# Kernel optimization log

Hardware: AMD Instinct MI355X
Metric: run time of the kernel (lower is better)

Reference implementation:

```python
import jax, jax.numpy as jnp
import numpy as np

N, E = 50000, 800000
IN, HID, OUT = 128, 256, 40
EPS = 1e-5


def setup_inputs() -> dict:
    key = jax.random.key(0)
    ks = jax.random.split(key, 16)
    def glorot(k, shape):
        lim = float(np.sqrt(6.0 / (shape[0] + shape[1])))
        return jax.random.uniform(k, shape, jnp.float32, -lim, lim)
    return {
        "x": jax.random.normal(ks[0], (N, IN), jnp.float32),
        "edge_index": jax.random.randint(ks[1], (2, E), 0, N, jnp.int64),
        "W1": glorot(ks[2], (IN, HID)),  "b1": jnp.zeros((HID,), jnp.float32),
        "g1": jnp.ones((HID,), jnp.float32), "be1": jnp.zeros((HID,), jnp.float32),
        "W2": glorot(ks[3], (HID, HID)), "b2": jnp.zeros((HID,), jnp.float32),
        "g2": jnp.ones((HID,), jnp.float32), "be2": jnp.zeros((HID,), jnp.float32),
        "W3": glorot(ks[4], (HID, OUT)), "b3": jnp.zeros((OUT,), jnp.float32),
        "Wl": glorot(ks[5], (OUT, OUT)), "bl": jnp.zeros((OUT,), jnp.float32),
    }


def _gcn_conv(h, src, dst, norm, W, b, n):
    # PyG GCNConv: transform, then normalized scatter-add over edges (+self-loops)
    m = h @ W                                     # [N, d_out]
    msg = m[src] * norm[:, None]                  # gather + edge scale
    out = jax.ops.segment_sum(msg, dst, num_segments=n)
    return out + b


def _bn(h, g, b):
    # BatchNorm1d (training-mode batch stats, biased variance)
    mu = jnp.mean(h, axis=0)
    var = jnp.var(h, axis=0)
    return (h - mu) * jax.lax.rsqrt(var + EPS) * g + b


def reference(x, edge_index, W1, b1, g1, be1, W2, b2, g2, be2, W3, b3, Wl, bl):
    n = x.shape[0]
    loops = jnp.arange(n, dtype=edge_index.dtype)
    src = jnp.concatenate([edge_index[0], loops])
    dst = jnp.concatenate([edge_index[1], loops])
    deg = jax.ops.segment_sum(jnp.ones(src.shape[0], x.dtype), dst, num_segments=n)
    dinv = jnp.where(deg > 0, jax.lax.rsqrt(deg), 0.0)
    norm = dinv[src] * dinv[dst]

    h = jax.nn.relu(_bn(_gcn_conv(x, src, dst, norm, W1, b1, n), g1, be1))
    h = jax.nn.relu(_bn(_gcn_conv(h, src, dst, norm, W2, b2, n), g2, be2))
    h = _gcn_conv(h, src, dst, norm, W3, b3, n)
    h = h @ Wl + bl
    return jax.nn.log_softmax(h, axis=1)
```

## Files before the change

kernel.cpp:

```cpp
#include <hip/hip_runtime.h>
#include <hip/hip_bf16.h>
#include <math.h>

#define IN_DIM 128
#define HID 256
#define OUT_DIM 40
#define OUT_PAD 64
#define CAP 64
#define EPS 1e-5f

typedef __attribute__((ext_vector_type(8))) short short8;
typedef __attribute__((ext_vector_type(4))) float floatx4;

__device__ __forceinline__ float b2f(unsigned short u) {
    union { unsigned int i; float f; } c; c.i = ((unsigned int)u) << 16; return c.f;
}
__device__ __forceinline__ unsigned short f2b(float f) {
    union { float f; unsigned int i; } c; c.f = f;
    unsigned int r = c.i + 0x7FFF + ((c.i >> 16) & 1);
    return (unsigned short)(r >> 16);
}

union U8 { uint4 u; unsigned short s[8]; };
union F8 { short8 v; unsigned short s[8]; uint4 u; };


__global__ void fill1_k(const int* __restrict__ src, const int* __restrict__ dst,
                        int* __restrict__ cnt, int* __restrict__ col2, int E,
                        const float* __restrict__ W1, const float* __restrict__ W2,
                        const float* __restrict__ W3, const float* __restrict__ Wl,
                        const float* __restrict__ b3, const float* __restrict__ bl,
                        unsigned short* __restrict__ W1t, unsigned short* __restrict__ W2t,
                        unsigned short* __restrict__ W3lt, float* __restrict__ bias2,
                        float* __restrict__ stats1, float* __restrict__ stats2) {
    if (blockIdx.x < 1024) {
        for (int e = blockIdx.x * 256 + threadIdx.x; e < E; e += 1024 * 256) {
            int d = dst[e];
            int p = atomicAdd(&cnt[d], 1);
            if (p < CAP) col2[d * CAP + p] = src[e];
        }
    } else if (blockIdx.x < 1536) {
        const int n1 = 256 * 128, n2 = 256 * 256;
        int j = (blockIdx.x - 1024) * 256 + threadIdx.x;
        if (j < n1) {
            int n = j >> 7, k = j & 127;
            W1t[j] = f2b(W1[k * 256 + n]);
        } else if (j < n1 + n2) {
            int j2 = j - n1;
            int n = j2 >> 8, k = j2 & 255;
            W2t[j2] = f2b(W2[k * 256 + n]);
        } else {
            int j3 = j - n1 - n2;
            int n = j3 >> 8, k = j3 & 255;
            float acc = 0.f;
            if (n < OUT_DIM) {
                for (int q = 0; q < OUT_DIM; ++q)
                    acc += W3[k * OUT_DIM + q] * Wl[q * OUT_DIM + n];
            }
            W3lt[j3] = (n < OUT_DIM) ? f2b(acc) : 0;
            if (j3 < OUT_DIM) {
                float b = bl[j3];
                for (int q = 0; q < OUT_DIM; ++q) b += b3[q] * Wl[q * OUT_DIM + j3];
                bias2[j3] = b;
            }
        }
    } else {
        int t = threadIdx.x;
        stats1[t] = 0.f; stats1[256 + t] = 0.f;
        stats2[t] = 0.f; stats2[256 + t] = 0.f;
    }
}


__global__ void conv_k(const float* __restrict__ x, const int* __restrict__ cnt,
                       float* __restrict__ dinv, unsigned short* __restrict__ xb, int N) {
    size_t nx = (size_t)N * 32;
    for (size_t i = blockIdx.x * 256 + threadIdx.x; i < nx; i += (size_t)1024 * 256) {
        size_t row = i >> 5;
        float dv = rsqrtf((float)(cnt[row] + 1));
        if ((i & 31) == 0) dinv[row] = dv;
        float4 v = ((const float4*)x)[i];
        ushort4 o;
        o.x = f2b(v.x * dv); o.y = f2b(v.y * dv);
        o.z = f2b(v.z * dv); o.w = f2b(v.w * dv);
        ((ushort4*)xb)[i] = o;
    }
}


template <bool BN>
__global__ __launch_bounds__(64, 3) void gemm_w(const unsigned short* __restrict__ A,
                                                const unsigned short* __restrict__ Bt,
                                                unsigned short* __restrict__ C,
                                                const float* __restrict__ rowscale,
                                                const float* __restrict__ bias,
                                                const float* __restrict__ bnstats,
                                                const float* __restrict__ g,
                                                const float* __restrict__ be,
                                                float invN,
                                                int M, int Nc, int K, int ldc) {
    __shared__ float s_sc[HID], s_sh[HID];
    int lane = threadIdx.x;
    if (BN) {
        for (int t = lane; t < K; t += 64) {
            float mu = bnstats[t] * invN;
            float var = bnstats[HID + t] * invN - mu * mu;
            float sc = g[t] * rsqrtf(var + EPS);
            s_sc[t] = sc;
            s_sh[t] = be[t] - mu * sc;
        }
        __syncthreads();
    }
    int r16 = lane & 15, quad = lane >> 4;
    int row0 = blockIdx.y * 64, col0 = blockIdx.x * 64;

    int arow[4];
#pragma unroll
    for (int mt = 0; mt < 4; ++mt) arow[mt] = min(row0 + mt * 16 + r16, M - 1);

    floatx4 acc[4][4] = {};

    for (int k0 = 0; k0 < K; k0 += 32) {
        int ka = k0 + quad * 8;
        F8 a[4], b[4];
#pragma unroll
        for (int mt = 0; mt < 4; ++mt)
            a[mt].u = *(const uint4*)&A[(size_t)arow[mt] * K + ka];
#pragma unroll
        for (int nt = 0; nt < 4; ++nt)
            b[nt].u = *(const uint4*)&Bt[(size_t)(col0 + nt * 16 + r16) * K + ka];
        if (BN) {
            float4 sc0 = *(const float4*)&s_sc[ka];
            float4 sc1 = *(const float4*)&s_sc[ka + 4];
            float4 sh0 = *(const float4*)&s_sh[ka];
            float4 sh1 = *(const float4*)&s_sh[ka + 4];
            float sc[8] = {sc0.x, sc0.y, sc0.z, sc0.w, sc1.x, sc1.y, sc1.z, sc1.w};
            float sh[8] = {sh0.x, sh0.y, sh0.z, sh0.w, sh1.x, sh1.y, sh1.z, sh1.w};
#pragma unroll
            for (int mt = 0; mt < 4; ++mt)
#pragma unroll
                for (int j = 0; j < 8; ++j) {
                    float f = b2f(a[mt].s[j]) * sc[j] + sh[j];
                    a[mt].s[j] = f2b(fmaxf(f, 0.f));
                }
        }
#pragma unroll
        for (int mt = 0; mt < 4; ++mt)
#pragma unroll
            for (int nt = 0; nt < 4; ++nt)
                acc[mt][nt] = __builtin_amdgcn_mfma_f32_16x16x32_bf16(a[mt].v, b[nt].v, acc[mt][nt], 0, 0, 0);
    }

#pragma unroll
    for (int mt = 0; mt < 4; ++mt) {
#pragma unroll
        for (int r = 0; r < 4; ++r) {
            int row = row0 + mt * 16 + quad * 4 + r;
            if (row >= M) continue;
            float dv = rowscale ? rowscale[row] : 1.f;
#pragma unroll
            for (int nt = 0; nt < 4; ++nt) {
                int colg = col0 + nt * 16 + r16;
                if (colg < Nc) {
                    float v = acc[mt][nt][r] * dv + (bias ? bias[colg] : 0.f);
                    C[(size_t)row * ldc + colg] = f2b(v);
                }
            }
        }
    }
}


__global__ __launch_bounds__(256, 8) void agg_h(const unsigned short* __restrict__ m,
                                                const int* __restrict__ col2,
                                                const int* __restrict__ cnt,
                                                const float* __restrict__ dinv,
                                                const float* __restrict__ bias,
                                                unsigned short* __restrict__ out,
                                                int N) {
    int v = blockIdx.x * 4 + (threadIdx.x >> 6);
    if (v >= N) return;
    int lane = threadIdx.x & 63;
    int half = lane >> 5;
    int c0 = (lane & 31) * 8;
    float dv = dinv[v];
    const int* col = col2 + v * CAP;
    int end = min(cnt[v], CAP);
    float a[8] = {};
    if (half == 0) {
        U8 r; r.u = *(const uint4*)&m[(size_t)v * HID + c0];
#pragma unroll
        for (int k = 0; k < 8; ++k) a[k] = b2f(r.s[k]);
    }
    int e = 0;
    for (; e + 8 <= end; e += 8) {
        int idx[4];
#pragma unroll
        for (int j = 0; j < 4; ++j) idx[j] = col[e + 2 * j + half];
        U8 rr[4];
#pragma unroll
        for (int j = 0; j < 4; ++j)
            rr[j].u = *(const uint4*)&m[(size_t)idx[j] * HID + c0];
#pragma unroll
        for (int j = 0; j < 4; ++j)
#pragma unroll
            for (int k = 0; k < 8; ++k) a[k] += b2f(rr[j].s[k]);
    }
    for (; e < end; e += 2) {
        int t = e + half;
        if (t < end) {
            U8 r; r.u = *(const uint4*)&m[(size_t)col[t] * HID + c0];
#pragma unroll
            for (int k = 0; k < 8; ++k) a[k] += b2f(r.s[k]);
        }
    }
#pragma unroll
    for (int k = 0; k < 8; ++k) a[k] += __shfl_xor(a[k], 32);
    if (half == 0) {
        U8 o;
#pragma unroll
        for (int k = 0; k < 8; ++k) o.s[k] = f2b(a[k] * dv + bias[c0 + k]);
        *(uint4*)&out[(size_t)v * HID + c0] = o.u;
    }
}

__global__ __launch_bounds__(256, 8) void agg_x(const unsigned short* __restrict__ m,
                                                const int* __restrict__ col2,
                                                const int* __restrict__ cnt,
                                                const float* __restrict__ dinv,
                                                unsigned short* __restrict__ out,
                                                int N) {
    int v = blockIdx.x * 4 + (threadIdx.x >> 6);
    if (v >= N) return;
    int lane = threadIdx.x & 63;
    int q = lane >> 4;
    int c0 = (lane & 15) * 8;
    float dv = dinv[v];
    const int* col = col2 + v * CAP;
    int end = min(cnt[v], CAP);
    float a[8] = {};
    if (q == 0) {
        U8 r; r.u = *(const uint4*)&m[(size_t)v * IN_DIM + c0];
#pragma unroll
        for (int k = 0; k < 8; ++k) a[k] = b2f(r.s[k]);
    }
    int e = 0;
    for (; e + 8 <= end; e += 8) {
        int idx[2];
#pragma unroll
        for (int j = 0; j < 2; ++j) idx[j] = col[e + 4 * j + q];
        U8 rr[2];
#pragma unroll
        for (int j = 0; j < 2; ++j)
            rr[j].u = *(const uint4*)&m[(size_t)idx[j] * IN_DIM + c0];
#pragma unroll
        for (int j = 0; j < 2; ++j)
#pragma unroll
            for (int k = 0; k < 8; ++k) a[k] += b2f(rr[j].s[k]);
    }
    for (; e < end; e += 4) {
        int t = e + q;
        if (t < end) {
            U8 r; r.u = *(const uint4*)&m[(size_t)col[t] * IN_DIM + c0];
#pragma unroll
            for (int k = 0; k < 8; ++k) a[k] += b2f(r.s[k]);
        }
    }
#pragma unroll
    for (int k = 0; k < 8; ++k) {
        a[k] += __shfl_xor(a[k], 16);
        a[k] += __shfl_xor(a[k], 32);
    }
    if (q == 0) {
        U8 o;
#pragma unroll
        for (int k = 0; k < 8; ++k) o.s[k] = f2b(a[k] * dv);
        *(uint4*)&out[(size_t)v * IN_DIM + c0] = o.u;
    }
}

__global__ __launch_bounds__(256, 8) void agg_o_ls(const unsigned short* __restrict__ m,
                                                   const int* __restrict__ col2,
                                                   const int* __restrict__ cnt,
                                                   const float* __restrict__ dinv,
                                                   const float* __restrict__ bias2,
                                                   float* __restrict__ out,
                                                   int N) {
    int v = blockIdx.x * 4 + (threadIdx.x >> 6);
    if (v >= N) return;
    int lane = threadIdx.x & 63;
    int slot = lane >> 3;
    int li = lane & 7;
    int c0 = li * 8;
    float dv = dinv[v];
    const int* col = col2 + v * CAP;
    int end = min(cnt[v], CAP);
    float a[8] = {};
    if (slot == 0) {
        U8 r; r.u = *(const uint4*)&m[(size_t)v * OUT_PAD + c0];
#pragma unroll
        for (int k = 0; k < 8; ++k) a[k] = b2f(r.s[k]);
    }
    int e = 0;
    for (; e + 16 <= end; e += 16) {
        int idx[2];
        idx[0] = col[e + slot];
        idx[1] = col[e + 8 + slot];
        U8 rr[2];
#pragma unroll
        for (int j = 0; j < 2; ++j)
            rr[j].u = *(const uint4*)&m[(size_t)idx[j] * OUT_PAD + c0];
#pragma unroll
        for (int j = 0; j < 2; ++j)
#pragma unroll
            for (int k = 0; k < 8; ++k) a[k] += b2f(rr[j].s[k]);
    }
    for (; e < end; e += 8) {
        int t = e + slot;
        if (t < end) {
            U8 r; r.u = *(const uint4*)&m[(size_t)col[t] * OUT_PAD + c0];
#pragma unroll
            for (int k = 0; k < 8; ++k) a[k] += b2f(r.s[k]);
        }
    }
#pragma unroll
    for (int k = 0; k < 8; ++k) {
        a[k] += __shfl_xor(a[k], 8);
        a[k] += __shfl_xor(a[k], 16);
        a[k] += __shfl_xor(a[k], 32);
    }
    bool valid = (li < 5);
    float mx = -INFINITY;
#pragma unroll
    for (int k = 0; k < 8; ++k) {
        float val = valid ? (a[k] * dv + bias2[c0 + k]) : -INFINITY;
        a[k] = val;
        mx = fmaxf(mx, val);
    }
    mx = fmaxf(mx, __shfl_xor(mx, 1));
    mx = fmaxf(mx, __shfl_xor(mx, 2));
    mx = fmaxf(mx, __shfl_xor(mx, 4));
    float s = 0.f;
    if (valid) {
#pragma unroll
        for (int k = 0; k < 8; ++k) s += expf(a[k] - mx);
    }
    s += __shfl_xor(s, 1);
    s += __shfl_xor(s, 2);
    s += __shfl_xor(s, 4);
    float ls = mx + logf(s);
    if (slot == 0 && valid) {
        float4 o0, o1;
        o0.x = a[0] - ls; o0.y = a[1] - ls; o0.z = a[2] - ls; o0.w = a[3] - ls;
        o1.x = a[4] - ls; o1.y = a[5] - ls; o1.z = a[6] - ls; o1.w = a[7] - ls;
        float* p = &out[(size_t)v * OUT_DIM + c0];
        *(float4*)p = o0;
        *(float4*)(p + 4) = o1;
    }
}


__global__ __launch_bounds__(256) void bn_stats(const unsigned short* __restrict__ h,
                                                float* __restrict__ stats, int N) {
    __shared__ float ls[8][2][256];
    int t = threadIdx.x;
    int walker = t >> 5;
    int c0 = (t & 31) * 8;
    int r0 = blockIdx.x * 128;
    int rend = min(r0 + 128, N);
    float s1[8] = {}, s2[8] = {};
    for (int r = r0 + walker; r < rend; r += 8) {
        U8 x; x.u = *(const uint4*)&h[(size_t)r * HID + c0];
#pragma unroll
        for (int k = 0; k < 8; ++k) {
            float v = b2f(x.s[k]);
            s1[k] += v; s2[k] += v * v;
        }
    }
#pragma unroll
    for (int k = 0; k < 8; ++k) {
        ls[walker][0][c0 + k] = s1[k];
        ls[walker][1][c0 + k] = s2[k];
    }
    __syncthreads();
    float a1 = 0.f, a2 = 0.f;
#pragma unroll
    for (int w = 0; w < 8; ++w) { a1 += ls[w][0][t]; a2 += ls[w][1][t]; }
    atomicAdd(&stats[t], a1);
    atomicAdd(&stats[HID + t], a2);
}


extern "C" void kernel_launch(void* const* d_in, const int* in_sizes, int n_in,
                              void* d_out, int out_size, void* d_ws, size_t ws_size,
                              hipStream_t stream) {
    const float* x   = (const float*)d_in[0];
    const int*  eidx = (const int*)d_in[1];
    const float* W1 = (const float*)d_in[2];
    const float* b1 = (const float*)d_in[3];
    const float* g1 = (const float*)d_in[4];
    const float* be1 = (const float*)d_in[5];
    const float* W2 = (const float*)d_in[6];
    const float* b2 = (const float*)d_in[7];
    const float* g2 = (const float*)d_in[8];
    const float* be2 = (const float*)d_in[9];
    const float* W3 = (const float*)d_in[10];
    const float* b3 = (const float*)d_in[11];
    const float* Wl = (const float*)d_in[12];
    const float* bl = (const float*)d_in[13];
    float* out = (float*)d_out;

    const int N = in_sizes[0] / IN_DIM;
    const int E = in_sizes[1] / 2;
    const int* src = eidx;
    const int* dst = eidx + E;

    size_t off = 0;
    char* ws = (char*)d_ws;
    auto carve = [&](size_t bytes) -> void* {
        void* p = ws + off;
        off += (bytes + 255) & ~(size_t)255;
        return p;
    };
    int*   cnt  = (int*)carve((size_t)N * 4);
    float* stats1 = (float*)carve((size_t)2 * HID * 4);
    float* stats2 = (float*)carve((size_t)2 * HID * 4);
    float* dinv = (float*)carve((size_t)N * 4);
    int*   col2 = (int*)carve((size_t)N * CAP * 4);
    unsigned short* xb   = (unsigned short*)carve((size_t)N * IN_DIM * 2);
    unsigned short* axb  = (unsigned short*)carve((size_t)N * IN_DIM * 2);
    unsigned short* W1t  = (unsigned short*)carve((size_t)256 * IN_DIM * 2);
    unsigned short* W2t  = (unsigned short*)carve((size_t)256 * HID * 2);
    unsigned short* W3lt = (unsigned short*)carve((size_t)128 * HID * 2);
    float* bias2 = (float*)carve((size_t)OUT_DIM * 4);
    unsigned short* mbuf = (unsigned short*)carve((size_t)N * HID * 2);
    unsigned short* hbuf = (unsigned short*)carve((size_t)N * HID * 2);

    hipMemsetAsync(cnt, 0, (size_t)N * 4, stream);
    fill1_k<<<1537, 256, 0, stream>>>(src, dst, cnt, col2, E,
                                      W1, W2, W3, Wl, b3, bl,
                                      W1t, W2t, W3lt, bias2, stats1, stats2);
    conv_k<<<1024, 256, 0, stream>>>(x, cnt, dinv, xb, N);

    int mb64 = (N + 63) / 64;
    int nodeBlocks = (N + 3) / 4;
    float invN = 1.f / (float)N;

    agg_x<<<nodeBlocks, 256, 0, stream>>>(xb, col2, cnt, dinv, axb, N);
    gemm_w<false><<<dim3(4, mb64), 64, 0, stream>>>(axb, W1t, hbuf, nullptr, b1,
                                                    nullptr, nullptr, nullptr,
                                                    invN, N, HID, IN_DIM, HID);
    bn_stats<<<(N + 127) / 128, 256, 0, stream>>>(hbuf, stats1, N);

    gemm_w<true><<<dim3(4, mb64), 64, 0, stream>>>(hbuf, W2t, mbuf, dinv, nullptr,
                                                   stats1, g1, be1,
                                                   invN, N, HID, HID, HID);
    agg_h<<<nodeBlocks, 256, 0, stream>>>(mbuf, col2, cnt, dinv, b2, hbuf, N);
    bn_stats<<<(N + 127) / 128, 256, 0, stream>>>(hbuf, stats2, N);

    gemm_w<true><<<dim3(1, mb64), 64, 0, stream>>>(hbuf, W3lt, mbuf, dinv, nullptr,
                                                   stats2, g2, be2,
                                                   invN, N, OUT_PAD, HID, OUT_PAD);
    agg_o_ls<<<nodeBlocks, 256, 0, stream>>>(mbuf, col2, cnt, dinv, bias2, out, N);
}
```

Measured before the change: 414.6 us.

## Fuse x conversion into setup kernel, BN1 stats into GEMM, smaller GEMM tiles

The separate conv_k pass is removed. The x-to-bf16 conversion now runs as extra blocks of the setup kernel, and the degree scaling is recomputed inside the aggregation kernels from cnt instead of reading a dinv array. The first GEMM now accumulates BatchNorm sums with shuffles and atomics, which removes one bn_stats pass. GEMM row tiles shrink to 32 and 16 rows and the launch-bounds occupancy target rises. The trade-offs are more atomic traffic, extra rsqrt work per gathered neighbour, and BN statistics taken from fp32 values before bf16 rounding.

Result: no change. 422.8 us (+2.0%).

```diff
diff --git a/kernel.cpp b/kernel.cpp
--- a/kernel.cpp
+++ b/kernel.cpp
@@ -32,7 +32,9 @@
                         const float* __restrict__ b3, const float* __restrict__ bl,
                         unsigned short* __restrict__ W1t, unsigned short* __restrict__ W2t,
                         unsigned short* __restrict__ W3lt, float* __restrict__ bias2,
-                        float* __restrict__ stats1, float* __restrict__ stats2) {
+                        float* __restrict__ stats1, float* __restrict__ stats2,
+                        const float* __restrict__ x, unsigned short* __restrict__ xb,
+                        int N) {
     if (blockIdx.x < 1024) {
         for (int e = blockIdx.x * 256 + threadIdx.x; e < E; e += 1024 * 256) {
             int d = dst[e];
@@ -64,42 +66,37 @@
                 bias2[j3] = b;
             }
         }
-    } else {
+    } else if (blockIdx.x == 1536) {
         int t = threadIdx.x;
         stats1[t] = 0.f; stats1[256 + t] = 0.f;
         stats2[t] = 0.f; stats2[256 + t] = 0.f;
-    }
-}
-
-
-__global__ void conv_k(const float* __restrict__ x, const int* __restrict__ cnt,
-                       float* __restrict__ dinv, unsigned short* __restrict__ xb, int N) {
-    size_t nx = (size_t)N * 32;
-    for (size_t i = blockIdx.x * 256 + threadIdx.x; i < nx; i += (size_t)1024 * 256) {
-        size_t row = i >> 5;
-        float dv = rsqrtf((float)(cnt[row] + 1));
-        if ((i & 31) == 0) dinv[row] = dv;
-        float4 v = ((const float4*)x)[i];
-        ushort4 o;
-        o.x = f2b(v.x * dv); o.y = f2b(v.y * dv);
-        o.z = f2b(v.z * dv); o.w = f2b(v.w * dv);
-        ((ushort4*)xb)[i] = o;
-    }
-}
-
-
-template <bool BN>
-__global__ __launch_bounds__(64, 3) void gemm_w(const unsigned short* __restrict__ A,
+    } else {
+        size_t nx = (size_t)N * 32;
+        size_t nbk = gridDim.x - 1537;
+        for (size_t i = (size_t)(blockIdx.x - 1537) * 256 + threadIdx.x; i < nx;
+             i += nbk * 256) {
+            float4 v = ((const float4*)x)[i];
+            ushort4 o;
+            o.x = f2b(v.x); o.y = f2b(v.y); o.z = f2b(v.z); o.w = f2b(v.w);
+            ((ushort4*)xb)[i] = o;
+        }
+    }
+}
+
+
+template <int MT, bool BN, bool STATS>
+__global__ __launch_bounds__(64, 6) void gemm_w(const unsigned short* __restrict__ A,
                                                 const unsigned short* __restrict__ Bt,
                                                 unsigned short* __restrict__ C,
-                                                const float* __restrict__ rowscale,
+                                                const int* __restrict__ cnt,
                                                 const float* __restrict__ bias,
                                                 const float* __restrict__ bnstats,
                                                 const float* __restrict__ g,
                                                 const float* __restrict__ be,
+                                                float* __restrict__ gstats,
                                                 float invN,
                                                 int M, int Nc, int K, int ldc) {
-    __shared__ float s_sc[HID], s_sh[HID];
+    __shared__ float s_sc[BN ? HID : 1], s_sh[BN ? HID : 1];
     int lane = threadIdx.x;
     if (BN) {
         for (int t = lane; t < K; t += 64) {
@@ -112,19 +109,19 @@
         __syncthreads();
     }
     int r16 = lane & 15, quad = lane >> 4;
-    int row0 = blockIdx.y * 64, col0 = blockIdx.x * 64;
-
-    int arow[4];
-#pragma unroll
-    for (int mt = 0; mt < 4; ++mt) arow[mt] = min(row0 + mt * 16 + r16, M - 1);
-
-    floatx4 acc[4][4] = {};
+    int row0 = blockIdx.y * (MT * 16), col0 = blockIdx.x * 64;
+
+    int arow[MT];
+#pragma unroll
+    for (int mt = 0; mt < MT; ++mt) arow[mt] = min(row0 + mt * 16 + r16, M - 1);
+
+    floatx4 acc[MT][4] = {};
 
     for (int k0 = 0; k0 < K; k0 += 32) {
         int ka = k0 + quad * 8;
-        F8 a[4], b[4];
-#pragma unroll
-        for (int mt = 0; mt < 4; ++mt)
+        F8 a[MT], b[4];
+#pragma unroll
+        for (int mt = 0; mt < MT; ++mt)
             a[mt].u = *(const uint4*)&A[(size_t)arow[mt] * K + ka];
 #pragma unroll
         for (int nt = 0; nt < 4; ++nt)
@@ -137,7 +134,7 @@
             float sc[8] = {sc0.x, sc0.y, sc0.z, sc0.w, sc1.x, sc1.y, sc1.z, sc1.w};
             float sh[8] = {sh0.x, sh0.y, sh0.z, sh0.w, sh1.x, sh1.y, sh1.z, sh1.w};
 #pragma unroll
-            for (int mt = 0; mt < 4; ++mt)
+            for (int mt = 0; mt < MT; ++mt)
 #pragma unroll
                 for (int j = 0; j < 8; ++j) {
                     float f = b2f(a[mt].s[j]) * sc[j] + sh[j];
@@ -145,36 +142,110 @@
                 }
         }
 #pragma unroll
-        for (int mt = 0; mt < 4; ++mt)
+        for (int mt = 0; mt < MT; ++mt)
 #pragma unroll
             for (int nt = 0; nt < 4; ++nt)
                 acc[mt][nt] = __builtin_amdgcn_mfma_f32_16x16x32_bf16(a[mt].v, b[nt].v, acc[mt][nt], 0, 0, 0);
     }
 
-#pragma unroll
-    for (int mt = 0; mt < 4; ++mt) {
+    float s1[4] = {0.f, 0.f, 0.f, 0.f}, s2[4] = {0.f, 0.f, 0.f, 0.f};
+#pragma unroll
+    for (int mt = 0; mt < MT; ++mt) {
 #pragma unroll
         for (int r = 0; r < 4; ++r) {
             int row = row0 + mt * 16 + quad * 4 + r;
             if (row >= M) continue;
-            float dv = rowscale ? rowscale[row] : 1.f;
+            float dv = cnt ? rsqrtf((float)(cnt[row] + 1)) : 1.f;
 #pragma unroll
             for (int nt = 0; nt < 4; ++nt) {
                 int colg = col0 + nt * 16 + r16;
                 if (colg < Nc) {
                     float v = acc[mt][nt][r] * dv + (bias ? bias[colg] : 0.f);
                     C[(size_t)row * ldc + colg] = f2b(v);
+                    if (STATS) { s1[nt] += v; s2[nt] += v * v; }
                 }
             }
         }
     }
-}
-
+    if (STATS) {
+#pragma unroll
+        for (int nt = 0; nt < 4; ++nt) {
+            s1[nt] += __shfl_xor(s1[nt], 16); s1[nt] += __shfl_xor(s1[nt], 32);
+            s2[nt] += __shfl_xor(s2[nt], 16); s2[nt] += __shfl_xor(s2[nt], 32);
+            if (quad == 0) {
+                int colg = col0 + nt * 16 + r16;
+                atomicAdd(&gstats[colg], s1[nt]);
+                atomicAdd(&gstats[HID + colg], s2[nt]);
+            }
+        }
+    }
+}
+
+
+__global__ __launch_bounds__(256, 8) void agg_x(const unsigned short* __restrict__ m,
+                                                const int* __restrict__ col2,
+                                                const int* __restrict__ cnt,
+                                                unsigned short* __restrict__ out,
+                                                int N) {
+    int v = blockIdx.x * 4 + (threadIdx.x >> 6);
+    if (v >= N) return;
+    int lane = threadIdx.x & 63;
+    int q = lane >> 4;
+    int c0 = (lane & 15) * 8;
+    int cv = cnt[v];
+    float dv = rsqrtf((float)(cv + 1));
+    const int* col = col2 + v * CAP;
+    int end = min(cv, CAP);
+    float a[8] = {};
+    {
+        U8 r; r.u = *(const uint4*)&m[(size_t)v * IN_DIM + c0];
+#pragma unroll
+        for (int k = 0; k < 8; ++k) a[k] = b2f(r.s[k]) * dv;
+    }
+    if (q != 0) { a[0]=a[1]=a[2]=a[3]=a[4]=a[5]=a[6]=a[7]=0.f; }
+    int e = 0;
+    for (; e + 8 <= end; e += 8) {
+        int idx[2];
+#pragma unroll
+        for (int j = 0; j < 2; ++j) idx[j] = col[e + 4 * j + q];
+        float ds[2];
+#pragma unroll
+        for (int j = 0; j < 2; ++j) ds[j] = rsqrtf((float)(cnt[idx[j]] + 1));
+        U8 rr[2];
+#pragma unroll
+        for (int j = 0; j < 2; ++j)
+            rr[j].u = *(const uint4*)&m[(size_t)idx[j] * IN_DIM + c0];
+#pragma unroll
+        for (int j = 0; j < 2; ++j)
+#pragma unroll
+            for (int k = 0; k < 8; ++k) a[k] += b2f(rr[j].s[k]) * ds[j];
+    }
+    for (; e < end; e += 4) {
+        int t = e + q;
+        if (t < end) {
+            int s = col[t];
+            float ds = rsqrtf((float)(cnt[s] + 1));
+            U8 r; r.u = *(const uint4*)&m[(size_t)s * IN_DIM + c0];
+#pragma unroll
+            for (int k = 0; k < 8; ++k) a[k] += b2f(r.s[k]) * ds;
+        }
+    }
+#pragma unroll
+    for (int k = 0; k < 8; ++k) {
+        a[k] += __shfl_xor(a[k], 16);
+        a[k] += __shfl_xor(a[k], 32);
+    }
+    if (q == 0) {
+        U8 o;
+#pragma unroll
+        for (int k = 0; k < 8; ++k) o.s[k] = f2b(a[k] * dv);
+        *(uint4*)&out[(size_t)v * IN_DIM + c0] = o.u;
+    }
+}
 
 __global__ __launch_bounds__(256, 8) void agg_h(const unsigned short* __restrict__ m,
                                                 const int* __restrict__ col2,
                                                 const int* __restrict__ cnt,
-                                                const float* __restrict__ dinv,
                                                 const float* __restrict__ bias,
                                                 unsigned short* __restrict__ out,
                                                 int N) {
@@ -183,9 +254,10 @@
     int lane = threadIdx.x & 63;
     int half = lane >> 5;
     int c0 = (lane & 31) * 8;
-    float dv = dinv[v];
+    int cv = cnt[v];
+    float dv = rsqrtf((float)(cv + 1));
     const int* col = col2 + v * CAP;
-    int end = min(cnt[v], CAP);
+    int end = min(cv, CAP);
     float a[8] = {};
     if (half == 0) {
         U8 r; r.u = *(const uint4*)&m[(size_t)v * HID + c0];
@@ -224,65 +296,9 @@
     }
 }
 
-__global__ __launch_bounds__(256, 8) void agg_x(const unsigned short* __restrict__ m,
-                                                const int* __restrict__ col2,
-                                                const int* __restrict__ cnt,
-                                                const float* __restrict__ dinv,
-                                                unsigned short* __restrict__ out,
-                                                int N) {
-    int v = blockIdx.x * 4 + (threadIdx.x >> 6);
-    if (v >= N) return;
-    int lane = threadIdx.x & 63;
-    int q = lane >> 4;
-    int c0 = (lane & 15) * 8;
-    float dv = dinv[v];
-    const int* col = col2 + v * CAP;
-    int end = min(cnt[v], CAP);
-    float a[8] = {};
-    if (q == 0) {
-        U8 r; r.u = *(const uint4*)&m[(size_t)v * IN_DIM + c0];
-#pragma unroll
-        for (int k = 0; k < 8; ++k) a[k] = b2f(r.s[k]);
-    }
-    int e = 0;
-    for (; e + 8 <= end; e += 8) {
-        int idx[2];
-#pragma unroll
-        for (int j = 0; j < 2; ++j) idx[j] = col[e + 4 * j + q];
-        U8 rr[2];
-#pragma unroll
-        for (int j = 0; j < 2; ++j)
-            rr[j].u = *(const uint4*)&m[(size_t)idx[j] * IN_DIM + c0];
-#pragma unroll
-        for (int j = 0; j < 2; ++j)
-#pragma unroll
-            for (int k = 0; k < 8; ++k) a[k] += b2f(rr[j].s[k]);
-    }
-    for (; e < end; e += 4) {
-        int t = e + q;
-        if (t < end) {
-            U8 r; r.u = *(const uint4*)&m[(size_t)col[t] * IN_DIM + c0];
-#pragma unroll
-            for (int k = 0; k < 8; ++k) a[k] += b2f(r.s[k]);
-        }
-    }
-#pragma unroll
-    for (int k = 0; k < 8; ++k) {
-        a[k] += __shfl_xor(a[k], 16);
-        a[k] += __shfl_xor(a[k], 32);
-    }
-    if (q == 0) {
-        U8 o;
-#pragma unroll
-        for (int k = 0; k < 8; ++k) o.s[k] = f2b(a[k] * dv);
-        *(uint4*)&out[(size_t)v * IN_DIM + c0] = o.u;
-    }
-}
-
 __global__ __launch_bounds__(256, 8) void agg_o_ls(const unsigned short* __restrict__ m,
                                                    const int* __restrict__ col2,
                                                    const int* __restrict__ cnt,
-                                                   const float* __restrict__ dinv,
                                                    const float* __restrict__ bias2,
                                                    float* __restrict__ out,
                                                    int N) {
@@ -292,9 +308,10 @@
     int slot = lane >> 3;
     int li = lane & 7;
     int c0 = li * 8;
-    float dv = dinv[v];
+    int cv = cnt[v];
+    float dv = rsqrtf((float)(cv + 1));
     const int* col = col2 + v * CAP;
-    int end = min(cnt[v], CAP);
+    int end = min(cv, CAP);
     float a[8] = {};
     if (slot == 0) {
         U8 r; r.u = *(const uint4*)&m[(size_t)v * OUT_PAD + c0];
@@ -425,7 +442,6 @@
     int*   cnt  = (int*)carve((size_t)N * 4);
     float* stats1 = (float*)carve((size_t)2 * HID * 4);
     float* stats2 = (float*)carve((size_t)2 * HID * 4);
-    float* dinv = (float*)carve((size_t)N * 4);
     int*   col2 = (int*)carve((size_t)N * CAP * 4);
     unsigned short* xb   = (unsigned short*)carve((size_t)N * IN_DIM * 2);
     unsigned short* axb  = (unsigned short*)carve((size_t)N * IN_DIM * 2);
@@ -437,29 +453,36 @@
     unsigned short* hbuf = (unsigned short*)carve((size_t)N * HID * 2);
 
     hipMemsetAsync(cnt, 0, (size_t)N * 4, stream);
-    fill1_k<<<1537, 256, 0, stream>>>(src, dst, cnt, col2, E,
-                                      W1, W2, W3, Wl, b3, bl,
-                                      W1t, W2t, W3lt, bias2, stats1, stats2);
-    conv_k<<<1024, 256, 0, stream>>>(x, cnt, dinv, xb, N);
-
-    int mb64 = (N + 63) / 64;
+    int xconvBlocks = (int)(((size_t)N * 32 + 255) / 256);
+    fill1_k<<<1537 + xconvBlocks, 256, 0, stream>>>(src, dst, cnt, col2, E,
+                                                    W1, W2, W3, Wl, b3, bl,
+                                                    W1t, W2t, W3lt, bias2,
+                                                    stats1, stats2, x, xb, N);
+
     int nodeBlocks = (N + 3) / 4;
     float invN = 1.f / (float)N;
-
-    agg_x<<<nodeBlocks, 256, 0, stream>>>(xb, col2, cnt, dinv, axb, N);
-    gemm_w<false><<<dim3(4, mb64), 64, 0, stream>>>(axb, W1t, hbuf, nullptr, b1,
-                                                    nullptr, nullptr, nullptr,
-                                                    invN, N, HID, IN_DIM, HID);
-    bn_stats<<<(N + 127) / 128, 256, 0, stream>>>(hbuf, stats1, N);
-
-    gemm_w<true><<<dim3(4, mb64), 64, 0, stream>>>(hbuf, W2t, mbuf, dinv, nullptr,
-                                                   stats1, g1, be1,
-                                                   invN, N, HID, HID, HID);
-    agg_h<<<nodeBlocks, 256, 0, stream>>>(mbuf, col2, cnt, dinv, b2, hbuf, N);
+    int mb32 = (N + 31) / 32;
+    int mb16 = (N + 15) / 16;
+
+    agg_x<<<nodeBlocks, 256, 0, stream>>>(xb, col2, cnt, axb, N);
+    gemm_w<2, false, true><<<dim3(4, mb32), 64, 0, stream>>>(axb, W1t, hbuf,
+                                                             nullptr, b1,
+                                                             nullptr, nullptr, nullptr,
+                                                             stats1, invN,
+                                                             N, HID, IN_DIM, HID);
+
+    gemm_w<2, true, false><<<dim3(4, mb32), 64, 0, stream>>>(hbuf, W2t, mbuf,
+                                                             cnt, nullptr,
+                                                             stats1, g1, be1,
+                                                             nullptr, invN,
+                                                             N, HID, HID, HID);
+    agg_h<<<nodeBlocks, 256, 0, stream>>>(mbuf, col2, cnt, b2, hbuf, N);
     bn_stats<<<(N + 127) / 128, 256, 0, stream>>>(hbuf, stats2, N);
 
-    gemm_w<true><<<dim3(1, mb64), 64, 0, stream>>>(hbuf, W3lt, mbuf, dinv, nullptr,
-                                                   stats2, g2, be2,
-                                                   invN, N, OUT_PAD, HID, OUT_PAD);
-    agg_o_ls<<<nodeBlocks, 256, 0, stream>>>(mbuf, col2, cnt, dinv, bias2, out, N);
-}
+    gemm_w<1, true, false><<<dim3(1, mb16), 64, 0, stream>>>(hbuf, W3lt, mbuf,
+                                                             cnt, nullptr,
+                                                             stats2, g2, be2,
+                                                             nullptr, invN,
+                                                             N, OUT_PAD, HID, OUT_PAD);
+    agg_o_ls<<<nodeBlocks, 256, 0, stream>>>(mbuf, col2, cnt, bias2, out, N);
+}
```
